# Kernel optimization log

Measured on AMD Instinct MI355X. Metric: run time of the kernel, lower is better.

Reference implementation:

```python
import jax, jax.numpy as jnp
import numpy as np

N_HEAD = 16
NEG_BIG = 1e10  # matches the torch module's -10000000000.0 additive mask


def setup_inputs() -> dict:
    key = jax.random.key(0)
    k1, k2, k3 = jax.random.split(key, 3)
    B, T, D = 2, 2048, 1024
    x = jax.random.normal(k1, (B, T, D), dtype=jnp.float32)
    W_attn = jax.random.normal(k2, (D, 3 * D), dtype=jnp.float32) * 0.02
    b_attn = jnp.zeros((3 * D,), dtype=jnp.float32)
    W_proj = jax.random.normal(k3, (D, D), dtype=jnp.float32) * 0.02
    b_proj = jnp.zeros((D,), dtype=jnp.float32)
    return {"x": x, "W_attn": W_attn, "b_attn": b_attn,
            "W_proj": W_proj, "b_proj": b_proj}


def reference(x, W_attn, b_attn, W_proj, b_proj):
    B, T, D = x.shape
    H = N_HEAD
    dh = D // H
    # c_attn: fused qkv projection
    qkv = x @ W_attn + b_attn                      # [B, T, 3D]
    q, k, v = jnp.split(qkv, 3, axis=-1)
    # split heads -> [B, H, T, dh]
    q = q.reshape(B, T, H, dh).transpose(0, 2, 1, 3)
    k = k.reshape(B, T, H, dh).transpose(0, 2, 1, 3)
    v = v.reshape(B, T, H, dh).transpose(0, 2, 1, 3)
    # scores [B, H, T, T]
    w = jnp.einsum("bhqd,bhkd->bhqk", q, k)
    w = w / jnp.sqrt(jnp.float32(dh))              # scale=True
    # causal additive mask: w*b - 1e10*(1-b), b = lower-triangular ones
    bias = jnp.tril(jnp.ones((T, T), dtype=w.dtype))
    w = w * bias - NEG_BIG * (1.0 - bias)
    w = jax.nn.softmax(w, axis=-1)
    a = jnp.einsum("bhqk,bhkd->bhqd", w, v)        # [B, H, T, dh]
    # merge heads
    a = a.transpose(0, 2, 1, 3).reshape(B, T, D)
    # c_proj
    return a @ W_proj + b_proj
```

## Files before the change

kernel.cpp:

```cpp
#include <hip/hip_runtime.h>
#include <hip/hip_bf16.h>


typedef unsigned short u16;
typedef unsigned int u32;
typedef __attribute__((ext_vector_type(4))) float f32x4;
typedef __attribute__((ext_vector_type(16))) float f32x16;
typedef __attribute__((ext_vector_type(8))) short bf16x8;
typedef __attribute__((ext_vector_type(4))) int i32x4;

__device__ __forceinline__ u16 f2bf(float f) {
  unsigned u = __builtin_bit_cast(unsigned, f);
  u += 0x7FFFu + ((u >> 16) & 1u);
  return (u16)(u >> 16);
}

__device__ __forceinline__ u32 cvtpk(float lo, float hi) {
  u32 r;
  asm("v_cvt_pk_bf16_f32 %0, %1, %2" : "=v"(r) : "v"(lo), "v"(hi));
  return r;
}

__device__ __forceinline__ void gl_lds16(const u16* g, u16* l) {
  __builtin_amdgcn_global_load_lds(
      (const __attribute__((address_space(1))) void*)g,
      (__attribute__((address_space(3))) void*)l, 16, 0, 0);
}

__global__ __launch_bounds__(256) void cast_bf16_kernel(const float* __restrict__ in,
                                                        u16* __restrict__ out, int n4) {
  int i = blockIdx.x * 256 + threadIdx.x;
  if (i < n4) {
    float4 f = reinterpret_cast<const float4*>(in)[i];
    ushort4 o;
    o.x = f2bf(f.x); o.y = f2bf(f.y); o.z = f2bf(f.z); o.w = f2bf(f.w);
    reinterpret_cast<ushort4*>(out)[i] = o;
  }
}

__global__ __launch_bounds__(256) void transpose_cast(const float* __restrict__ in,
                                                      u16* __restrict__ out, int R, int C) {
  __shared__ float tile[32][33];
  const int c0 = blockIdx.x * 32, r0 = blockIdx.y * 32;
  const int tx = threadIdx.x, ty = threadIdx.y;
#pragma unroll
  for (int i = 0; i < 4; ++i)
    tile[ty + 8 * i][tx] = in[(size_t)(r0 + ty + 8 * i) * C + c0 + tx];
  __syncthreads();
#pragma unroll
  for (int i = 0; i < 4; ++i)
    out[(size_t)(c0 + ty + 8 * i) * R + r0 + tx] = f2bf(tile[tx][ty + 8 * i]);
}

template <int MODE>
__global__ __launch_bounds__(256) void gemm_bf16(
    const u16* __restrict__ A, const u16* __restrict__ Bt, const float* __restrict__ bias,
    float* __restrict__ outF, u16* __restrict__ Qh, u16* __restrict__ Kh, u16* __restrict__ Vh,
    int N, int K) {
  __shared__ u16 As[128 * 32];
  __shared__ u16 Bs[128 * 32];
  const int tid = threadIdx.x;
  const int wave = tid >> 6, lane = tid & 63;
  const int kg = lane >> 4, rr = lane & 15;
  const int wm = wave >> 1, wn = wave & 1;
  const int nwg = gridDim.x * gridDim.y;
  const int lin = blockIdx.y * gridDim.x + blockIdx.x;
  const int swz = (lin & 7) * (nwg >> 3) + (lin >> 3);
  const int bx = swz % gridDim.x, by = swz / gridDim.x;
  const int rowA0 = by * 128, colB0 = bx * 128;

  const f32x4 z4 = {0.f, 0.f, 0.f, 0.f};
  f32x4 acc[4][4];
#pragma unroll
  for (int i = 0; i < 4; ++i)
#pragma unroll
    for (int j = 0; j < 4; ++j) acc[i][j] = z4;

  const int r_st = tid >> 2;
  const int c_st = (tid & 3) * 8;

  for (int k0 = 0; k0 < K; k0 += 32) {
#pragma unroll
    for (int i = 0; i < 2; ++i) {
      gl_lds16(A + (size_t)(rowA0 + i * 64 + r_st) * K + k0 + c_st,
               As + (i * 256 + (wave << 6)) * 8);
      gl_lds16(Bt + (size_t)(colB0 + i * 64 + r_st) * K + k0 + c_st,
               Bs + (i * 256 + (wave << 6)) * 8);
    }
    __syncthreads();

    bf16x8 af[4], bfr[4];
#pragma unroll
    for (int mi = 0; mi < 4; ++mi)
      af[mi] = *reinterpret_cast<const bf16x8*>(&As[(wm * 64 + mi * 16 + rr) * 32 + kg * 8]);
#pragma unroll
    for (int ni = 0; ni < 4; ++ni)
      bfr[ni] = *reinterpret_cast<const bf16x8*>(&Bs[(wn * 64 + ni * 16 + rr) * 32 + kg * 8]);
#pragma unroll
    for (int mi = 0; mi < 4; ++mi)
#pragma unroll
      for (int ni = 0; ni < 4; ++ni)
        acc[mi][ni] = __builtin_amdgcn_mfma_f32_16x16x32_bf16(af[mi], bfr[ni], acc[mi][ni], 0, 0, 0);
    __syncthreads();
  }

  const float QS = 0.125f * 1.44269504088896f;
#pragma unroll
  for (int mi = 0; mi < 4; ++mi) {
#pragma unroll
    for (int ni = 0; ni < 4; ++ni) {
      const int col = colB0 + wn * 64 + ni * 16 + rr;
      const float bcol = bias[col];
      f32x4 a = acc[mi][ni];
#pragma unroll
      for (int v = 0; v < 4; ++v) {
        const int row = rowA0 + wm * 64 + mi * 16 + kg * 4 + v;
        const float val = a[v] + bcol;
        if (MODE == 1) {
          outF[(size_t)row * N + col] = val;
        } else {
          const int b = row >> 11, t = row & 2047;
          const int which = col >> 10, d = col & 1023;
          const int h = d >> 6, dd = d & 63;
          const size_t idx = (((size_t)(b * 16 + h)) * 2048 + t) * 64 + dd;
          if (which == 0)
            Qh[idx] = f2bf(val * QS);
          else if (which == 1)
            Kh[idx] = f2bf(val);
          else
            Vh[idx] = f2bf(val);
        }
      }
    }
  }
}

__global__ __launch_bounds__(256) void transpose_v(const u16* __restrict__ Vh,
                                                   u16* __restrict__ VhT) {
  __shared__ u16 tile[64][72];
  const int tid = threadIdx.x;
  const int t0 = blockIdx.x * 64;
  const int bh = blockIdx.y;
  const u16* src = Vh + ((size_t)bh * 2048 + t0) * 64;
  {
    const int ty = tid >> 2, tx = (tid & 3) * 16;
    *reinterpret_cast<bf16x8*>(&tile[ty][tx]) =
        *reinterpret_cast<const bf16x8*>(src + ty * 64 + tx);
    *reinterpret_cast<bf16x8*>(&tile[ty][tx + 8]) =
        *reinterpret_cast<const bf16x8*>(src + ty * 64 + tx + 8);
  }
  __syncthreads();
  {
    const int dd = tid >> 2, toff = (tid & 3) * 16;
    bf16x8 v0, v1;
#pragma unroll
    for (int j = 0; j < 8; ++j) v0[j] = (short)tile[toff + j][dd];
#pragma unroll
    for (int j = 0; j < 8; ++j) v1[j] = (short)tile[toff + 8 + j][dd];
    u16* dst = VhT + ((size_t)bh * 64 + dd) * 2048 + t0 + toff;
    *reinterpret_cast<bf16x8*>(dst) = v0;
    *reinterpret_cast<bf16x8*>(dst + 8) = v1;
  }
}

__global__ __launch_bounds__(256) void attn_fwd(const u16* __restrict__ Qh,
                                                const u16* __restrict__ Kh,
                                                const u16* __restrict__ VhT,
                                                u16* __restrict__ Ab) {
  __shared__ u16 Olq[4][32][72];
  __shared__ float Ml[4][2][32];
  const int tid = threadIdx.x;
  const int wave = tid >> 6, lane = tid & 63;
  const int lq = lane & 31, hi = lane >> 5;
  const int blk = blockIdx.x;
  const int qi = blk >> 5;
  const int bh = blk & 31;
  const int qtile = 63 - qi;
  const int q0 = qtile * 32;
  const int myq = q0 + lq;
  const size_t kvbase = (size_t)bh * 2048;

  const int n64 = (q0 + 32 + 63) >> 6;
  const int base = n64 >> 2, rem = n64 & 3;
  const int cnt = base + (wave < rem ? 1 : 0);
  const int start = wave * base + (wave < rem ? wave : rem);

  bf16x8 qf[4];
  {
    const u16* qptr = Qh + (kvbase + q0 + lq) * 64 + hi * 8;
#pragma unroll
    for (int ks = 0; ks < 4; ++ks)
      qf[ks] = *reinterpret_cast<const bf16x8*>(qptr + ks * 16);
  }

  f32x16 oA, oB;
#pragma unroll
  for (int i = 0; i < 16; ++i) { oA[i] = 0.f; oB[i] = 0.f; }
  float m = -1e30f, l = 0.f;

  for (int kvb = start; kvb < start + cnt; ++kvb) {
    const int kv0 = kvb * 64;

    const u16* kptr = Kh + (kvbase + kv0 + lq) * 64 + hi * 8;
    bf16x8 kfA[4], kfB[4];
#pragma unroll
    for (int ks = 0; ks < 4; ++ks) {
      kfA[ks] = *reinterpret_cast<const bf16x8*>(kptr + ks * 16);
      kfB[ks] = *reinterpret_cast<const bf16x8*>(kptr + 2048 + ks * 16);
    }

    f32x16 sA, sB;
#pragma unroll
    for (int i = 0; i < 16; ++i) { sA[i] = 0.f; sB[i] = 0.f; }
    __builtin_amdgcn_s_setprio(1);
#pragma unroll
    for (int ks = 0; ks < 4; ++ks)
      sA = __builtin_amdgcn_mfma_f32_32x32x16_bf16(kfA[ks], qf[ks], sA, 0, 0, 0);
#pragma unroll
    for (int ks = 0; ks < 4; ++ks)
      sB = __builtin_amdgcn_mfma_f32_32x32x16_bf16(kfB[ks], qf[ks], sB, 0, 0, 0);
    __builtin_amdgcn_s_setprio(0);

    if (kvb == n64 - 1) {
#pragma unroll
      for (int r = 0; r < 16; ++r) {
        const int kvA = kv0 + (r & 3) + 8 * (r >> 2) + 4 * hi;
        if (kvA > myq) sA[r] = -1e30f;
        if (kvA + 32 > myq) sB[r] = -1e30f;
      }
    }

    float pmax = -1e30f;
#pragma unroll
    for (int r = 0; r < 16; ++r) pmax = fmaxf(pmax, fmaxf(sA[r], sB[r]));
    pmax = fmaxf(pmax, __shfl_xor(pmax, 32));
    if (!__all(pmax - m <= 8.0f)) {
      const float mn = fmaxf(m, pmax);
      const float sc = __builtin_amdgcn_exp2f(m - mn);
      l *= sc;
      oA *= sc;
      oB *= sc;
      m = mn;
    }
    float rsum = 0.f;
#pragma unroll
    for (int r = 0; r < 16; ++r) {
      const float pa = __builtin_amdgcn_exp2f(sA[r] - m);
      const float pb = __builtin_amdgcn_exp2f(sB[r] - m);
      sA[r] = pa; sB[r] = pb;
      rsum += pa + pb;
    }
    rsum += __shfl_xor(rsum, 32);
    l += rsum;

    const u16* vptr = VhT + ((size_t)bh * 64 + lq) * 2048 + kv0 + hi * 8;
    bf16x8 vfA[4], vfB[4];
#pragma unroll
    for (int ks = 0; ks < 4; ++ks) {
      vfA[ks] = *reinterpret_cast<const bf16x8*>(vptr + ks * 16);
      vfB[ks] = *reinterpret_cast<const bf16x8*>(vptr + 32 * 2048 + ks * 16);
    }

    u32 pkA[8], pkB[8];
#pragma unroll
    for (int i = 0; i < 8; ++i) {
      pkA[i] = cvtpk(sA[2 * i], sA[2 * i + 1]);
      pkB[i] = cvtpk(sB[2 * i], sB[2 * i + 1]);
    }
    bf16x8 pf[4];
    {
      auto w0 = __builtin_amdgcn_permlane32_swap(pkA[0], pkA[2], false, false);
      auto w1 = __builtin_amdgcn_permlane32_swap(pkA[1], pkA[3], false, false);
      i32x4 t0 = {(int)w0[0], (int)w1[0], (int)w0[1], (int)w1[1]};
      pf[0] = __builtin_bit_cast(bf16x8, t0);
      auto w2 = __builtin_amdgcn_permlane32_swap(pkA[4], pkA[6], false, false);
      auto w3 = __builtin_amdgcn_permlane32_swap(pkA[5], pkA[7], false, false);
      i32x4 t1 = {(int)w2[0], (int)w3[0], (int)w2[1], (int)w3[1]};
      pf[1] = __builtin_bit_cast(bf16x8, t1);
      auto w4 = __builtin_amdgcn_permlane32_swap(pkB[0], pkB[2], false, false);
      auto w5 = __builtin_amdgcn_permlane32_swap(pkB[1], pkB[3], false, false);
      i32x4 t2 = {(int)w4[0], (int)w5[0], (int)w4[1], (int)w5[1]};
      pf[2] = __builtin_bit_cast(bf16x8, t2);
      auto w6 = __builtin_amdgcn_permlane32_swap(pkB[4], pkB[6], false, false);
      auto w7 = __builtin_amdgcn_permlane32_swap(pkB[5], pkB[7], false, false);
      i32x4 t3 = {(int)w6[0], (int)w7[0], (int)w6[1], (int)w7[1]};
      pf[3] = __builtin_bit_cast(bf16x8, t3);
    }

    __builtin_amdgcn_s_setprio(1);
#pragma unroll
    for (int ks = 0; ks < 4; ++ks)
      oA = __builtin_amdgcn_mfma_f32_32x32x16_bf16(vfA[ks], pf[ks], oA, 0, 0, 0);
#pragma unroll
    for (int ks = 0; ks < 4; ++ks)
      oB = __builtin_amdgcn_mfma_f32_32x32x16_bf16(vfB[ks], pf[ks], oB, 0, 0, 0);
    __builtin_amdgcn_s_setprio(0);
  }

  if (hi == 0) {
    Ml[wave][0][lq] = m;
    Ml[wave][1][lq] = l;
  }
  {
    u32* orow = reinterpret_cast<u32*>(&Olq[wave][lq][0]);
#pragma unroll
    for (int qd = 0; qd < 4; ++qd) {
      const int dh0 = 8 * qd + 4 * hi;
      orow[(dh0 >> 1) + 0] = cvtpk(oA[4 * qd + 0], oA[4 * qd + 1]);
      orow[(dh0 >> 1) + 1] = cvtpk(oA[4 * qd + 2], oA[4 * qd + 3]);
      orow[((dh0 + 32) >> 1) + 0] = cvtpk(oB[4 * qd + 0], oB[4 * qd + 1]);
      orow[((dh0 + 32) >> 1) + 1] = cvtpk(oB[4 * qd + 2], oB[4 * qd + 3]);
    }
  }
  __syncthreads();

  const int col = tid >> 3;
  const int dh0 = (tid & 7) * 8;
  float M = -1e30f;
  float mw[4];
#pragma unroll
  for (int w = 0; w < 4; ++w) { mw[w] = Ml[w][0][col]; M = fmaxf(M, mw[w]); }
  float lsum = 0.f;
  float scw[4];
#pragma unroll
  for (int w = 0; w < 4; ++w) {
    scw[w] = __builtin_amdgcn_exp2f(mw[w] - M);
    lsum += scw[w] * Ml[w][1][col];
  }
  const float inv = 1.0f / lsum;
  float acc8[8];
#pragma unroll
  for (int i = 0; i < 8; ++i) acc8[i] = 0.f;
#pragma unroll
  for (int w = 0; w < 4; ++w) {
    bf16x8 ov = *reinterpret_cast<const bf16x8*>(&Olq[w][col][dh0]);
#pragma unroll
    for (int i = 0; i < 8; ++i) {
      const float f = __builtin_bit_cast(float, ((u32)(u16)ov[i]) << 16);
      acc8[i] += scw[w] * f;
    }
  }
  const int b = bh >> 4, h = bh & 15;
  bf16x8 outv;
#pragma unroll
  for (int i = 0; i < 8; ++i) outv[i] = (short)f2bf(acc8[i] * inv);
  *reinterpret_cast<bf16x8*>(Ab + ((size_t)b * 2048 + q0 + col) * 1024 + h * 64 + dh0) = outv;
}

extern "C" void kernel_launch(void* const* d_in, const int* in_sizes, int n_in,
                              void* d_out, int out_size, void* d_ws, size_t ws_size,
                              hipStream_t stream) {
  const float* x      = (const float*)d_in[0];
  const float* W_attn = (const float*)d_in[1];
  const float* b_attn = (const float*)d_in[2];
  const float* W_proj = (const float*)d_in[3];
  const float* b_proj = (const float*)d_in[4];
  float* out = (float*)d_out;

  u16* xb  = (u16*)d_ws;
  u16* Wat = xb + (size_t)4096 * 1024;
  u16* Wpt = Wat + (size_t)3072 * 1024;
  u16* Qh  = Wpt + (size_t)1024 * 1024;
  u16* Kh  = Qh + (size_t)4194304;
  u16* VhT = Kh + (size_t)4194304;
  u16* Ab  = VhT + (size_t)4194304;
  u16* Vh  = Ab;

  cast_bf16_kernel<<<4096, 256, 0, stream>>>(x, xb, 4096 * 1024 / 4);
  transpose_cast<<<dim3(96, 32), dim3(32, 8), 0, stream>>>(W_attn, Wat, 1024, 3072);
  transpose_cast<<<dim3(32, 32), dim3(32, 8), 0, stream>>>(W_proj, Wpt, 1024, 1024);
  gemm_bf16<0><<<dim3(24, 32), 256, 0, stream>>>(xb, Wat, b_attn, nullptr, Qh, Kh, Vh,
                                                 3072, 1024);
  transpose_v<<<dim3(32, 32), 256, 0, stream>>>(Vh, VhT);
  attn_fwd<<<dim3(2048), 256, 0, stream>>>(Qh, Kh, VhT, Ab);
  gemm_bf16<1><<<dim3(8, 32), 256, 0, stream>>>(Ab, Wpt, b_proj, out, nullptr, nullptr, nullptr,
                                                1024, 1024);
}
```

Measured before the change: 227.3 us.

## Double-buffer K loads in attention and split projection GEMM into smaller tiles

The attention inner loop is restructured into a ping-pong scheme: the K fragments for the next KV block are prefetched into a second register set while the current block is computed, and the V loads are issued at the start of each step. The kernel also gets a launch bound asking for two blocks per CU, and the LDS output row stride is padded from 72 to 80. The output projection GEMM gets its own kernel with 128x64 tiles, giving 512 workgroups instead of 256 to fill more CUs. The extra K register set raises register pressure and may conflict with the two-blocks-per-CU occupancy target.

```diff
diff --git a/kernel.cpp b/kernel.cpp
--- a/kernel.cpp
+++ b/kernel.cpp
@@ -52,11 +52,9 @@
     out[(size_t)(c0 + ty + 8 * i) * R + r0 + tx] = f2bf(tile[tx][ty + 8 * i]);
 }
 
-template <int MODE>
-__global__ __launch_bounds__(256) void gemm_bf16(
+__global__ __launch_bounds__(256) void gemm_qkv(
     const u16* __restrict__ A, const u16* __restrict__ Bt, const float* __restrict__ bias,
-    float* __restrict__ outF, u16* __restrict__ Qh, u16* __restrict__ Kh, u16* __restrict__ Vh,
-    int N, int K) {
+    u16* __restrict__ Qh, u16* __restrict__ Kh, u16* __restrict__ Vh, int K) {
   __shared__ u16 As[128 * 32];
   __shared__ u16 Bs[128 * 32];
   const int tid = threadIdx.x;
@@ -116,20 +114,79 @@
       for (int v = 0; v < 4; ++v) {
         const int row = rowA0 + wm * 64 + mi * 16 + kg * 4 + v;
         const float val = a[v] + bcol;
-        if (MODE == 1) {
-          outF[(size_t)row * N + col] = val;
-        } else {
-          const int b = row >> 11, t = row & 2047;
-          const int which = col >> 10, d = col & 1023;
-          const int h = d >> 6, dd = d & 63;
-          const size_t idx = (((size_t)(b * 16 + h)) * 2048 + t) * 64 + dd;
-          if (which == 0)
-            Qh[idx] = f2bf(val * QS);
-          else if (which == 1)
-            Kh[idx] = f2bf(val);
-          else
-            Vh[idx] = f2bf(val);
-        }
+        const int b = row >> 11, t = row & 2047;
+        const int which = col >> 10, d = col & 1023;
+        const int h = d >> 6, dd = d & 63;
+        const size_t idx = (((size_t)(b * 16 + h)) * 2048 + t) * 64 + dd;
+        if (which == 0)
+          Qh[idx] = f2bf(val * QS);
+        else if (which == 1)
+          Kh[idx] = f2bf(val);
+        else
+          Vh[idx] = f2bf(val);
+      }
+    }
+  }
+}
+
+__global__ __launch_bounds__(256) void gemm_proj(
+    const u16* __restrict__ A, const u16* __restrict__ Bt, const float* __restrict__ bias,
+    float* __restrict__ outF, int N, int K) {
+  __shared__ u16 As[128 * 32];
+  __shared__ u16 Bs[64 * 32];
+  const int tid = threadIdx.x;
+  const int wave = tid >> 6, lane = tid & 63;
+  const int kg = lane >> 4, rr = lane & 15;
+  const int nwg = gridDim.x * gridDim.y;
+  const int lin = blockIdx.y * gridDim.x + blockIdx.x;
+  const int swz = (lin & 7) * (nwg >> 3) + (lin >> 3);
+  const int bx = swz % gridDim.x, by = swz / gridDim.x;
+  const int rowA0 = by * 128, colB0 = bx * 64;
+
+  const f32x4 z4 = {0.f, 0.f, 0.f, 0.f};
+  f32x4 acc[2][4];
+#pragma unroll
+  for (int i = 0; i < 2; ++i)
+#pragma unroll
+    for (int j = 0; j < 4; ++j) acc[i][j] = z4;
+
+  const int r_st = tid >> 2;
+  const int c_st = (tid & 3) * 8;
+
+  for (int k0 = 0; k0 < K; k0 += 32) {
+#pragma unroll
+    for (int i = 0; i < 2; ++i)
+      gl_lds16(A + (size_t)(rowA0 + i * 64 + r_st) * K + k0 + c_st,
+               As + (i * 256 + (wave << 6)) * 8);
+    gl_lds16(Bt + (size_t)(colB0 + r_st) * K + k0 + c_st, Bs + (wave << 6) * 8);
+    __syncthreads();
+
+    bf16x8 af[2], bfr[4];
+#pragma unroll
+    for (int mi = 0; mi < 2; ++mi)
+      af[mi] = *reinterpret_cast<const bf16x8*>(&As[(wave * 32 + mi * 16 + rr) * 32 + kg * 8]);
+#pragma unroll
+    for (int ni = 0; ni < 4; ++ni)
+      bfr[ni] = *reinterpret_cast<const bf16x8*>(&Bs[(ni * 16 + rr) * 32 + kg * 8]);
+#pragma unroll
+    for (int mi = 0; mi < 2; ++mi)
+#pragma unroll
+      for (int ni = 0; ni < 4; ++ni)
+        acc[mi][ni] = __builtin_amdgcn_mfma_f32_16x16x32_bf16(af[mi], bfr[ni], acc[mi][ni], 0, 0, 0);
+    __syncthreads();
+  }
+
+#pragma unroll
+  for (int mi = 0; mi < 2; ++mi) {
+#pragma unroll
+    for (int ni = 0; ni < 4; ++ni) {
+      const int col = colB0 + ni * 16 + rr;
+      const float bcol = bias[col];
+      f32x4 a = acc[mi][ni];
+#pragma unroll
+      for (int v = 0; v < 4; ++v) {
+        const int row = rowA0 + wave * 32 + mi * 16 + kg * 4 + v;
+        outF[(size_t)row * N + col] = a[v] + bcol;
       }
     }
   }
@@ -163,11 +220,112 @@
   }
 }
 
-__global__ __launch_bounds__(256) void attn_fwd(const u16* __restrict__ Qh,
-                                                const u16* __restrict__ Kh,
-                                                const u16* __restrict__ VhT,
-                                                u16* __restrict__ Ab) {
-  __shared__ u16 Olq[4][32][72];
+__device__ __forceinline__ void load_k(const u16* kptr, bf16x8 (&kA)[4], bf16x8 (&kB)[4]) {
+#pragma unroll
+  for (int ks = 0; ks < 4; ++ks) {
+    kA[ks] = *reinterpret_cast<const bf16x8*>(kptr + ks * 16);
+    kB[ks] = *reinterpret_cast<const bf16x8*>(kptr + 2048 + ks * 16);
+  }
+}
+
+__device__ __forceinline__ void attn_step(
+    int kvb, int n64, int myq, int hi, const u16* vbase,
+    const bf16x8 (&qf)[4], const bf16x8 (&kA)[4], const bf16x8 (&kB)[4],
+    f32x16& oA, f32x16& oB, float& m, float& l) {
+  bf16x8 vfA[4], vfB[4];
+  const u16* vp = vbase + kvb * 64;
+#pragma unroll
+  for (int ks = 0; ks < 4; ++ks) {
+    vfA[ks] = *reinterpret_cast<const bf16x8*>(vp + ks * 16);
+    vfB[ks] = *reinterpret_cast<const bf16x8*>(vp + 32 * 2048 + ks * 16);
+  }
+
+  f32x16 sA, sB;
+#pragma unroll
+  for (int i = 0; i < 16; ++i) { sA[i] = 0.f; sB[i] = 0.f; }
+  __builtin_amdgcn_s_setprio(1);
+#pragma unroll
+  for (int ks = 0; ks < 4; ++ks)
+    sA = __builtin_amdgcn_mfma_f32_32x32x16_bf16(kA[ks], qf[ks], sA, 0, 0, 0);
+#pragma unroll
+  for (int ks = 0; ks < 4; ++ks)
+    sB = __builtin_amdgcn_mfma_f32_32x32x16_bf16(kB[ks], qf[ks], sB, 0, 0, 0);
+  __builtin_amdgcn_s_setprio(0);
+
+  if (kvb == n64 - 1) {
+    const int kv0 = kvb * 64;
+#pragma unroll
+    for (int r = 0; r < 16; ++r) {
+      const int kvA = kv0 + (r & 3) + 8 * (r >> 2) + 4 * hi;
+      if (kvA > myq) sA[r] = -1e30f;
+      if (kvA + 32 > myq) sB[r] = -1e30f;
+    }
+  }
+
+  float pmax = -1e30f;
+#pragma unroll
+  for (int r = 0; r < 16; ++r) pmax = fmaxf(pmax, fmaxf(sA[r], sB[r]));
+  pmax = fmaxf(pmax, __shfl_xor(pmax, 32));
+  if (!__all(pmax - m <= 8.0f)) {
+    const float mn = fmaxf(m, pmax);
+    const float sc = __builtin_amdgcn_exp2f(m - mn);
+    l *= sc;
+    oA *= sc;
+    oB *= sc;
+    m = mn;
+  }
+  float rsum = 0.f;
+#pragma unroll
+  for (int r = 0; r < 16; ++r) {
+    const float pa = __builtin_amdgcn_exp2f(sA[r] - m);
+    const float pb = __builtin_amdgcn_exp2f(sB[r] - m);
+    sA[r] = pa; sB[r] = pb;
+    rsum += pa + pb;
+  }
+  rsum += __shfl_xor(rsum, 32);
+  l += rsum;
+
+  u32 pkA[8], pkB[8];
+#pragma unroll
+  for (int i = 0; i < 8; ++i) {
+    pkA[i] = cvtpk(sA[2 * i], sA[2 * i + 1]);
+    pkB[i] = cvtpk(sB[2 * i], sB[2 * i + 1]);
+  }
+  bf16x8 pf[4];
+  {
+    auto w0 = __builtin_amdgcn_permlane32_swap(pkA[0], pkA[2], false, false);
+    auto w1 = __builtin_amdgcn_permlane32_swap(pkA[1], pkA[3], false, false);
+    i32x4 t0 = {(int)w0[0], (int)w1[0], (int)w0[1], (int)w1[1]};
+    pf[0] = __builtin_bit_cast(bf16x8, t0);
+    auto w2 = __builtin_amdgcn_permlane32_swap(pkA[4], pkA[6], false, false);
+    auto w3 = __builtin_amdgcn_permlane32_swap(pkA[5], pkA[7], false, false);
+    i32x4 t1 = {(int)w2[0], (int)w3[0], (int)w2[1], (int)w3[1]};
+    pf[1] = __builtin_bit_cast(bf16x8, t1);
+    auto w4 = __builtin_amdgcn_permlane32_swap(pkB[0], pkB[2], false, false);
+    auto w5 = __builtin_amdgcn_permlane32_swap(pkB[1], pkB[3], false, false);
+    i32x4 t2 = {(int)w4[0], (int)w5[0], (int)w4[1], (int)w5[1]};
+    pf[2] = __builtin_bit_cast(bf16x8, t2);
+    auto w6 = __builtin_amdgcn_permlane32_swap(pkB[4], pkB[6], false, false);
+    auto w7 = __builtin_amdgcn_permlane32_swap(pkB[5], pkB[7], false, false);
+    i32x4 t3 = {(int)w6[0], (int)w7[0], (int)w6[1], (int)w7[1]};
+    pf[3] = __builtin_bit_cast(bf16x8, t3);
+  }
+
+  __builtin_amdgcn_s_setprio(1);
+#pragma unroll
+  for (int ks = 0; ks < 4; ++ks)
+    oA = __builtin_amdgcn_mfma_f32_32x32x16_bf16(vfA[ks], pf[ks], oA, 0, 0, 0);
+#pragma unroll
+  for (int ks = 0; ks < 4; ++ks)
+    oB = __builtin_amdgcn_mfma_f32_32x32x16_bf16(vfB[ks], pf[ks], oB, 0, 0, 0);
+  __builtin_amdgcn_s_setprio(0);
+}
+
+__global__ __launch_bounds__(256, 2) void attn_fwd(const u16* __restrict__ Qh,
+                                                   const u16* __restrict__ Kh,
+                                                   const u16* __restrict__ VhT,
+                                                   u16* __restrict__ Ab) {
+  __shared__ u16 Olq[4][32][80];
   __shared__ float Ml[4][2][32];
   const int tid = threadIdx.x;
   const int wave = tid >> 6, lane = tid & 63;
@@ -184,6 +342,7 @@
   const int base = n64 >> 2, rem = n64 & 3;
   const int cnt = base + (wave < rem ? 1 : 0);
   const int start = wave * base + (wave < rem ? wave : rem);
+  const int end = start + cnt;
 
   bf16x8 qf[4];
   {
@@ -198,103 +357,21 @@
   for (int i = 0; i < 16; ++i) { oA[i] = 0.f; oB[i] = 0.f; }
   float m = -1e30f, l = 0.f;
 
-  for (int kvb = start; kvb < start + cnt; ++kvb) {
-    const int kv0 = kvb * 64;
-
-    const u16* kptr = Kh + (kvbase + kv0 + lq) * 64 + hi * 8;
-    bf16x8 kfA[4], kfB[4];
-#pragma unroll
-    for (int ks = 0; ks < 4; ++ks) {
-      kfA[ks] = *reinterpret_cast<const bf16x8*>(kptr + ks * 16);
-      kfB[ks] = *reinterpret_cast<const bf16x8*>(kptr + 2048 + ks * 16);
-    }
-
-    f32x16 sA, sB;
-#pragma unroll
-    for (int i = 0; i < 16; ++i) { sA[i] = 0.f; sB[i] = 0.f; }
-    __builtin_amdgcn_s_setprio(1);
-#pragma unroll
-    for (int ks = 0; ks < 4; ++ks)
-      sA = __builtin_amdgcn_mfma_f32_32x32x16_bf16(kfA[ks], qf[ks], sA, 0, 0, 0);
-#pragma unroll
-    for (int ks = 0; ks < 4; ++ks)
-      sB = __builtin_amdgcn_mfma_f32_32x32x16_bf16(kfB[ks], qf[ks], sB, 0, 0, 0);
-    __builtin_amdgcn_s_setprio(0);
-
-    if (kvb == n64 - 1) {
-#pragma unroll
-      for (int r = 0; r < 16; ++r) {
-        const int kvA = kv0 + (r & 3) + 8 * (r >> 2) + 4 * hi;
-        if (kvA > myq) sA[r] = -1e30f;
-        if (kvA + 32 > myq) sB[r] = -1e30f;
-      }
-    }
-
-    float pmax = -1e30f;
-#pragma unroll
-    for (int r = 0; r < 16; ++r) pmax = fmaxf(pmax, fmaxf(sA[r], sB[r]));
-    pmax = fmaxf(pmax, __shfl_xor(pmax, 32));
-    if (!__all(pmax - m <= 8.0f)) {
-      const float mn = fmaxf(m, pmax);
-      const float sc = __builtin_amdgcn_exp2f(m - mn);
-      l *= sc;
-      oA *= sc;
-      oB *= sc;
-      m = mn;
-    }
-    float rsum = 0.f;
-#pragma unroll
-    for (int r = 0; r < 16; ++r) {
-      const float pa = __builtin_amdgcn_exp2f(sA[r] - m);
-      const float pb = __builtin_amdgcn_exp2f(sB[r] - m);
-      sA[r] = pa; sB[r] = pb;
-      rsum += pa + pb;
-    }
-    rsum += __shfl_xor(rsum, 32);
-    l += rsum;
-
-    const u16* vptr = VhT + ((size_t)bh * 64 + lq) * 2048 + kv0 + hi * 8;
-    bf16x8 vfA[4], vfB[4];
-#pragma unroll
-    for (int ks = 0; ks < 4; ++ks) {
-      vfA[ks] = *reinterpret_cast<const bf16x8*>(vptr + ks * 16);
-      vfB[ks] = *reinterpret_cast<const bf16x8*>(vptr + 32 * 2048 + ks * 16);
-    }
-
-    u32 pkA[8], pkB[8];
-#pragma unroll
-    for (int i = 0; i < 8; ++i) {
-      pkA[i] = cvtpk(sA[2 * i], sA[2 * i + 1]);
-      pkB[i] = cvtpk(sB[2 * i], sB[2 * i + 1]);
-    }
-    bf16x8 pf[4];
-    {
-      auto w0 = __builtin_amdgcn_permlane32_swap(pkA[0], pkA[2], false, false);
-      auto w1 = __builtin_amdgcn_permlane32_swap(pkA[1], pkA[3], false, false);
-      i32x4 t0 = {(int)w0[0], (int)w1[0], (int)w0[1], (int)w1[1]};
-      pf[0] = __builtin_bit_cast(bf16x8, t0);
-      auto w2 = __builtin_amdgcn_permlane32_swap(pkA[4], pkA[6], false, false);
-      auto w3 = __builtin_amdgcn_permlane32_swap(pkA[5], pkA[7], false, false);
-      i32x4 t1 = {(int)w2[0], (int)w3[0], (int)w2[1], (int)w3[1]};
-      pf[1] = __builtin_bit_cast(bf16x8, t1);
-      auto w4 = __builtin_amdgcn_permlane32_swap(pkB[0], pkB[2], false, false);
-      auto w5 = __builtin_amdgcn_permlane32_swap(pkB[1], pkB[3], false, false);
-      i32x4 t2 = {(int)w4[0], (int)w5[0], (int)w4[1], (int)w5[1]};
-      pf[2] = __builtin_bit_cast(bf16x8, t2);
-      auto w6 = __builtin_amdgcn_permlane32_swap(pkB[4], pkB[6], false, false);
-      auto w7 = __builtin_amdgcn_permlane32_swap(pkB[5], pkB[7], false, false);
-      i32x4 t3 = {(int)w6[0], (int)w7[0], (int)w6[1], (int)w7[1]};
-      pf[3] = __builtin_bit_cast(bf16x8, t3);
-    }
-
-    __builtin_amdgcn_s_setprio(1);
-#pragma unroll
-    for (int ks = 0; ks < 4; ++ks)
-      oA = __builtin_amdgcn_mfma_f32_32x32x16_bf16(vfA[ks], pf[ks], oA, 0, 0, 0);
-#pragma unroll
-    for (int ks = 0; ks < 4; ++ks)
-      oB = __builtin_amdgcn_mfma_f32_32x32x16_bf16(vfB[ks], pf[ks], oB, 0, 0, 0);
-    __builtin_amdgcn_s_setprio(0);
+  const u16* kbase = Kh + (kvbase + lq) * 64 + hi * 8;
+  const u16* vbase = VhT + ((size_t)bh * 64 + lq) * 2048 + hi * 8;
+
+  bf16x8 kA0[4], kB0[4], kA1[4], kB1[4];
+  int kvb = start;
+  if (kvb < end) {
+    load_k(kbase + (size_t)kvb * 4096, kA0, kB0);
+    while (true) {
+      if (kvb + 1 < end) load_k(kbase + (size_t)(kvb + 1) * 4096, kA1, kB1);
+      attn_step(kvb, n64, myq, hi, vbase, qf, kA0, kB0, oA, oB, m, l);
+      if (++kvb >= end) break;
+      if (kvb + 1 < end) load_k(kbase + (size_t)(kvb + 1) * 4096, kA0, kB0);
+      attn_step(kvb, n64, myq, hi, vbase, qf, kA1, kB1, oA, oB, m, l);
+      if (++kvb >= end) break;
+    }
   }
 
   if (hi == 0) {
@@ -369,10 +446,8 @@
   cast_bf16_kernel<<<4096, 256, 0, stream>>>(x, xb, 4096 * 1024 / 4);
   transpose_cast<<<dim3(96, 32), dim3(32, 8), 0, stream>>>(W_attn, Wat, 1024, 3072);
   transpose_cast<<<dim3(32, 32), dim3(32, 8), 0, stream>>>(W_proj, Wpt, 1024, 1024);
-  gemm_bf16<0><<<dim3(24, 32), 256, 0, stream>>>(xb, Wat, b_attn, nullptr, Qh, Kh, Vh,
-                                                 3072, 1024);
+  gemm_qkv<<<dim3(24, 32), 256, 0, stream>>>(xb, Wat, b_attn, Qh, Kh, Vh, 1024);
   transpose_v<<<dim3(32, 32), 256, 0, stream>>>(Vh, VhT);
   attn_fwd<<<dim3(2048), 256, 0, stream>>>(Qh, Kh, VhT, Ab);
-  gemm_bf16<1><<<dim3(8, 32), 256, 0, stream>>>(Ab, Wpt, b_proj, out, nullptr, nullptr, nullptr,
-                                                1024, 1024);
-}
+  gemm_proj<<<dim3(16, 32), 256, 0, stream>>>(Ab, Wpt, b_proj, out, 1024, 1024);
+}
```

Result: faster. 218.2 us (-4.0%).
